# Optimization experiments

Measured on AMD Instinct MI355X. Metric: run time of the kernel, lower is better.

Reference implementation:

```python
import jax, jax.numpy as jnp
import numpy as np

EPS_COS = 1e-8   # torch cosine_similarity eps
EPS_DEN = 1e-6   # denominator eps in original loss
TEMP = 0.1


def setup_inputs() -> dict:
    key = jax.random.key(0)
    k1, _ = jax.random.split(key)
    N, D = 16384, 2048
    x = jax.random.normal(k1, (N, D), dtype=jnp.float32)
    pos_pair = jnp.arange(2, dtype=jnp.int64)  # (i, j) = (0, 1), i != j
    return {"x": x, "pos_pair": pos_pair}


def reference(x, pos_pair):
    # x: [N, D]; pos_pair: [2] int indices (i, j)
    i = pos_pair[0]
    j = pos_pair[1]
    xi = x[i]                                        # [D] anchor
    # cosine similarity of anchor against every row (single fused matvec)
    dots = x @ xi                                    # [N]
    norms = jnp.maximum(jnp.linalg.norm(x, axis=1), EPS_COS)   # [N]
    ni = jnp.maximum(jnp.linalg.norm(xi), EPS_COS)
    cos = dots / (norms * ni)                        # [N]
    e = jnp.exp(cos / TEMP)                          # [N]
    # denominator sums over all k != i (k == j included, as in original)
    mask = jnp.arange(x.shape[0]) != i
    denominator = jnp.sum(jnp.where(mask, e, 0.0))
    nominator = e[j]
    loss = -jnp.log(nominator / (denominator + EPS_DEN))
    return loss.reshape(1)  # original returns shape [1]
```

## Files before the change

kernel.cpp:

```cpp
#include <hip/hip_runtime.h>
#include <math.h>

#define D 2048
#define EPS_COS 1e-8f
#define EPS_DEN 1e-6f
#define INV_TEMP 10.0f
#define TPB 256
#define WPB 4
#define RPW 4

__device__ __forceinline__ void get_ij(const int* __restrict__ p, int n,
                                       int& i, int& j) {
    int i32 = p[0], j32 = p[1];
    if (i32 >= 0 && i32 < n && j32 >= 0 && j32 < n && i32 != j32) {
        i = i32; j = j32; return;
    }
    const long long* p64 = (const long long*)p;
    i = (int)p64[0]; j = (int)p64[1];
}

__global__ __launch_bounds__(TPB)
void e_kernel(const float* __restrict__ x, const int* __restrict__ pos,
              float* __restrict__ part, float* __restrict__ nom, int n) {
    int i, j;
    get_ij(pos, n, i, j);
    const int lane  = threadIdx.x & 63;
    const int wave  = threadIdx.x >> 6;
    const int gwave = blockIdx.x * WPB + wave;
    const int row0  = gwave * RPW;

    const float4* __restrict__ xi = (const float4*)(x + (size_t)i * D);

    float4 b[8], a[2][8];
    const float4* __restrict__ p0 = (const float4*)(x + (size_t)row0 * D);
#pragma unroll
    for (int w = 0; w < 8; ++w) a[0][w] = p0[lane + w * 64];
#pragma unroll
    for (int w = 0; w < 8; ++w) b[w] = xi[lane + w * 64];

    float sqi = 0.f;
#pragma unroll
    for (int w = 0; w < 8; ++w)
        sqi = fmaf(b[w].x, b[w].x, fmaf(b[w].y, b[w].y,
              fmaf(b[w].z, b[w].z, fmaf(b[w].w, b[w].w, sqi))));
#pragma unroll
    for (int off = 32; off; off >>= 1) sqi += __shfl_down(sqi, off);
    const float ni = fmaxf(sqrtf(sqi), EPS_COS);

    float den_local = 0.f, ej = 0.f;

#pragma unroll
    for (int r = 0; r < RPW; ++r) {
        if (r + 1 < RPW) {
            const float4* __restrict__ pn =
                (const float4*)(x + (size_t)(row0 + r + 1) * D);
#pragma unroll
            for (int w = 0; w < 8; ++w) a[(r + 1) & 1][w] = pn[lane + w * 64];
        }
        float dot = 0.f, sq = 0.f;
#pragma unroll
        for (int w = 0; w < 8; ++w) {
            float4 c = a[r & 1][w];
            dot = fmaf(c.x, b[w].x, fmaf(c.y, b[w].y,
                  fmaf(c.z, b[w].z, fmaf(c.w, b[w].w, dot))));
            sq  = fmaf(c.x, c.x, fmaf(c.y, c.y,
                  fmaf(c.z, c.z, fmaf(c.w, c.w, sq))));
        }
#pragma unroll
        for (int off = 32; off; off >>= 1) {
            dot += __shfl_down(dot, off);
            sq  += __shfl_down(sq,  off);
        }
        if (lane == 0) {
            const int row = row0 + r;
            float e = expf(INV_TEMP * dot / (fmaxf(sqrtf(sq), EPS_COS) * ni));
            if (row != i) den_local += e;
            if (row == j) ej = e;
        }
    }

    __shared__ float s_den[WPB];
    if (lane == 0) {
        s_den[wave] = den_local;
        if (ej != 0.f) *nom = ej;
    }
    __syncthreads();
    if (threadIdx.x == 0)
        part[blockIdx.x] = (s_den[0] + s_den[1]) + (s_den[2] + s_den[3]);
}

__global__ __launch_bounds__(256)
void loss_kernel(const float* __restrict__ part, const float* __restrict__ nom,
                 float* __restrict__ out, int nblk) {
    const int t = threadIdx.x;
    float s = 0.f;
    if (t < nblk / 4) {
        float4 v = ((const float4*)part)[t];
        s = (v.x + v.y) + (v.z + v.w);
    }
#pragma unroll
    for (int off = 32; off; off >>= 1) s += __shfl_down(s, off);

    __shared__ float ls[4];
    if ((t & 63) == 0) ls[t >> 6] = s;
    __syncthreads();

    if (t == 0) {
        float den = (ls[0] + ls[1]) + (ls[2] + ls[3]);
        out[0] = -logf(nom[0] / (den + EPS_DEN));
    }
}

extern "C" void kernel_launch(void* const* d_in, const int* in_sizes, int n_in,
                              void* d_out, int out_size, void* d_ws, size_t ws_size,
                              hipStream_t stream) {
    const float* x    = (const float*)d_in[0];
    const int*   pos  = (const int*)d_in[1];
    float*       out  = (float*)d_out;

    const int n    = in_sizes[0] / D;
    const int nblk = n / (WPB * RPW);

    float* part = (float*)d_ws;
    float* nom  = (float*)d_ws + nblk;

    e_kernel<<<nblk, TPB, 0, stream>>>(x, pos, part, nom, n);
    loss_kernel<<<1, 256, 0, stream>>>(part, nom, out, nblk);
}
```

Baseline: 189.9 us.

## Fuse final loss reduction into main kernel via atomics and last-block finalize

Replaces the two-kernel scheme (per-block partials plus a single-block loss kernel) with one kernel. Each block atomically adds its denominator partial into one of 64 slots, and the last block to finish, found through an atomic counter, computes the loss. Blocks grow to 512 threads with 8 rows per wave, giving 256 blocks. A memset is added to zero the accumulators. The intent is to remove a kernel launch and its tail, at the cost of an extra memset, atomics, and fewer, larger blocks that may lower occupancy or memory parallelism. The odd NaN-pattern check used to size the counter increment looks fragile.

```diff
diff --git a/kernel.cpp b/kernel.cpp
--- a/kernel.cpp
+++ b/kernel.cpp
@@ -5,9 +5,11 @@
 #define EPS_COS 1e-8f
 #define EPS_DEN 1e-6f
 #define INV_TEMP 10.0f
-#define TPB 256
-#define WPB 4
-#define RPW 4
+#define TPB 512
+#define WPB 8
+#define RPW 8
+#define NBLK 256
+#define NSLOT 64
 
 __device__ __forceinline__ void get_ij(const int* __restrict__ p, int n,
                                        int& i, int& j) {
@@ -20,8 +22,9 @@
 }
 
 __global__ __launch_bounds__(TPB)
-void e_kernel(const float* __restrict__ x, const int* __restrict__ pos,
-              float* __restrict__ part, float* __restrict__ nom, int n) {
+void fused_kernel(const float* __restrict__ x, const int* __restrict__ pos,
+                  float* __restrict__ out, float* __restrict__ accf,
+                  unsigned* __restrict__ accu, int n) {
     int i, j;
     get_ij(pos, n, i, j);
     const int lane  = threadIdx.x & 63;
@@ -79,35 +82,31 @@
         }
     }
 
-    __shared__ float s_den[WPB];
+    __shared__ float s_den[WPB], s_ej[WPB];
     if (lane == 0) {
         s_den[wave] = den_local;
-        if (ej != 0.f) *nom = ej;
+        s_ej[wave]  = ej;
     }
     __syncthreads();
-    if (threadIdx.x == 0)
-        part[blockIdx.x] = (s_den[0] + s_den[1]) + (s_den[2] + s_den[3]);
-}
 
-__global__ __launch_bounds__(256)
-void loss_kernel(const float* __restrict__ part, const float* __restrict__ nom,
-                 float* __restrict__ out, int nblk) {
-    const int t = threadIdx.x;
-    float s = 0.f;
-    if (t < nblk / 4) {
-        float4 v = ((const float4*)part)[t];
-        s = (v.x + v.y) + (v.z + v.w);
-    }
+    if (threadIdx.x == 0) {
+        float bden = 0.f, bej = 0.f;
 #pragma unroll
-    for (int off = 32; off; off >>= 1) s += __shfl_down(s, off);
-
-    __shared__ float ls[4];
-    if ((t & 63) == 0) ls[t >> 6] = s;
-    __syncthreads();
-
-    if (t == 0) {
-        float den = (ls[0] + ls[1]) + (ls[2] + ls[3]);
-        out[0] = -logf(nom[0] / (den + EPS_DEN));
+        for (int w = 0; w < WPB; ++w) { bden += s_den[w]; bej += s_ej[w]; }
+        float r1 = atomicAdd(&accf[blockIdx.x & (NSLOT - 1)], bden);
+        float r2 = (bej != 0.f) ? atomicAdd(&accf[NSLOT], bej) : 0.f;
+        unsigned inc = 1u
+            + ((__float_as_uint(r1) == 0x7F800001u) ? 1u : 0u)
+            + ((__float_as_uint(r2) == 0x7F800001u) ? 1u : 0u);
+        asm volatile("s_waitcnt vmcnt(0)" ::: "memory");
+        unsigned old = atomicAdd(accu, inc);
+        if (old == (unsigned)(NBLK - 1)) {
+            float den = 0.f;
+#pragma unroll
+            for (int s = 0; s < NSLOT; ++s) den += atomicAdd(&accf[s], 0.f);
+            float nom = atomicAdd(&accf[NSLOT], 0.f);
+            out[0] = -logf(nom / (den + EPS_DEN));
+        }
     }
 }
 
@@ -117,13 +116,11 @@
     const float* x    = (const float*)d_in[0];
     const int*   pos  = (const int*)d_in[1];
     float*       out  = (float*)d_out;
+    float*       accf = (float*)d_ws;
+    unsigned*    accu = (unsigned*)d_ws + NSLOT + 1;
 
-    const int n    = in_sizes[0] / D;
-    const int nblk = n / (WPB * RPW);
+    const int n = in_sizes[0] / D;
 
-    float* part = (float*)d_ws;
-    float* nom  = (float*)d_ws + nblk;
-
-    e_kernel<<<nblk, TPB, 0, stream>>>(x, pos, part, nom, n);
-    loss_kernel<<<1, 256, 0, stream>>>(part, nom, out, nblk);
+    hipMemsetAsync(d_ws, 0, (NSLOT + 2) * sizeof(float), stream);
+    fused_kernel<<<NBLK, TPB, 0, stream>>>(x, pos, out, accf, accu, n);
 }
```

Result: slower. 215.2 us (+13.3%).
